# Performance work log

Measured on AMD Instinct MI355X. Metric: run time of the kernel, lower is better.

The kernel has to match this reference:

```python
import jax, jax.numpy as jnp
import numpy as np
import math

BS, SL, NE, NH = 4, 2048, 1024, 16
HD = NE // NH  # 64


def setup_inputs() -> dict:
    key = jax.random.key(0)
    ks = jax.random.split(key, 5)
    x = jax.random.normal(ks[0], (BS, SL, NE), dtype=jnp.float32)
    # causal mask: 1 where attending allowed (j <= i), 0 otherwise
    mask = jnp.tril(jnp.ones((SL, SL), dtype=jnp.int32))[None, None, :, :]
    s = 1.0 / math.sqrt(NE)
    Wqkv = jax.random.normal(ks[1], (NE, 3 * NE), dtype=jnp.float32) * s
    bqkv = jax.random.normal(ks[2], (3 * NE,), dtype=jnp.float32) * 0.02
    Wo = jax.random.normal(ks[3], (NE, NE), dtype=jnp.float32) * s
    bo = jax.random.normal(ks[4], (NE,), dtype=jnp.float32) * 0.02
    return {"x": x, "mask": mask, "Wqkv": Wqkv, "bqkv": bqkv, "Wo": Wo, "bo": bo}


def reference(x, mask, Wqkv, bqkv, Wo, bo):
    bs, sl, ne = x.shape
    qkv = x @ Wqkv + bqkv                       # [bs, sl, 3*ne]
    q, k, v = jnp.split(qkv, 3, axis=-1)
    # [bs, sl, ne] -> [bs, nh, sl, hd]
    q = q.reshape(bs, sl, NH, HD).transpose(0, 2, 1, 3)
    k = k.reshape(bs, sl, NH, HD).transpose(0, 2, 1, 3)
    v = v.reshape(bs, sl, NH, HD).transpose(0, 2, 1, 3)
    scale = 1.0 / math.sqrt(HD)
    att = jnp.einsum('bhqd,bhkd->bhqk', q, k) * scale  # [bs, nh, sl, sl]
    att = jnp.where(mask == 0, -jnp.inf, att)
    w = jax.nn.softmax(att, axis=-1)
    y = jnp.einsum('bhqk,bhkd->bhqd', w, v)            # [bs, nh, sl, hd]
    y = y.transpose(0, 2, 1, 3).reshape(bs, sl, ne)
    return y @ Wo + bo
```

## Files before the change

### kernel.cpp

```cpp
#include <hip/hip_runtime.h>

#define BS 4
#define SL 2048
#define NE 1024
#define NH 16
#define HD 64
#define N3 3072

typedef __attribute__((ext_vector_type(8))) __bf16 bf16x8;
typedef __attribute__((ext_vector_type(4))) float f32x4;
typedef __attribute__((ext_vector_type(4))) short s16x4;
typedef unsigned short u16;

#define CE 0.18033688011112042f

#if __has_builtin(__builtin_amdgcn_exp2f)
#define EXP2(x) __builtin_amdgcn_exp2f(x)
#else
#define EXP2(x) exp2f(x)
#endif

__device__ __forceinline__ u16 f2bf(float f) {
  union { float f; unsigned int u; } v; v.f = f;
  unsigned int r = v.u + 0x7FFFu + ((v.u >> 16) & 1u);
  return (u16)(r >> 16);
}

__device__ __forceinline__ int permpack(float a, float b) {
  return __builtin_amdgcn_perm(__float_as_uint(b), __float_as_uint(a),
                               0x07060302u);
}

__device__ __forceinline__ void gld16(const void* g, void* l) {
#if __has_builtin(__builtin_amdgcn_global_load_lds)
  __builtin_amdgcn_global_load_lds(
      (const __attribute__((address_space(1))) unsigned int*)g,
      (__attribute__((address_space(3))) unsigned int*)l, 16, 0, 0);
#else
  *(int4*)((char*)l + (size_t)(threadIdx.x & 63) * 16) = *(const int4*)g;
#endif
}

template <int N>
__device__ __forceinline__ void vmw() {
  if constexpr (N == 0)
    asm volatile("s_waitcnt vmcnt(0)" ::: "memory");
  else if constexpr (N == 4)
    asm volatile("s_waitcnt vmcnt(4)" ::: "memory");
}

__global__ void convert_x(const float* __restrict__ x, u16* __restrict__ xb) {
  int i = (blockIdx.x * 256 + threadIdx.x) * 8;
  float4 f0 = *(const float4*)(x + i);
  float4 f1 = *(const float4*)(x + i + 4);
  union { int4 v; u16 h[8]; } p;
  p.h[0] = f2bf(f0.x); p.h[1] = f2bf(f0.y);
  p.h[2] = f2bf(f0.z); p.h[3] = f2bf(f0.w);
  p.h[4] = f2bf(f1.x); p.h[5] = f2bf(f1.y);
  p.h[6] = f2bf(f1.z); p.h[7] = f2bf(f1.w);
  *(int4*)(xb + i) = p.v;
}

__global__ void transpose_w(const float* __restrict__ W, u16* __restrict__ Wt,
                            int K, int N) {
  __shared__ u16 tile[32][33];
  int bn = blockIdx.x * 32, bk = blockIdx.y * 32;
  int tx = threadIdx.x, ty = threadIdx.y;
  for (int r = 0; r < 32; r += 8)
    tile[ty + r][tx] = f2bf(W[(size_t)(bk + ty + r) * N + bn + tx]);
  __syncthreads();
  for (int r = 0; r < 32; r += 8)
    Wt[(size_t)(bn + ty + r) * K + bk + tx] = tile[tx][ty + r];
}

#define MFMA_G(a, b, c) \
  __builtin_amdgcn_mfma_f32_16x16x32_bf16(a, b, c, 0, 0, 0)
#define GBAR()                         \
  do {                                 \
    __builtin_amdgcn_s_barrier();      \
    __builtin_amdgcn_sched_barrier(0); \
  } while (0)

template <int C32, int SCALEQ>
__global__ __launch_bounds__(256, 3) void gemm3b(
    const u16* __restrict__ A, const u16* __restrict__ Bt,
    const float* __restrict__ bias, void* __restrict__ C, int M, int N, int K,
    int lda) {
  constexpr int BM = 128, BN = 128, BK = 32;
  constexpr int TSZ = BM * BK;
  __shared__ u16 As[3][TSZ];
  __shared__ u16 Bs[3][TSZ];

  const int tid = threadIdx.x;
  const int w = tid >> 6, lane = tid & 63;
  const int lq = lane >> 4, lr = lane & 15;
  const int nwx = gridDim.x;
  const int nwg = nwx * gridDim.y;
  const int lin = blockIdx.y * nwx + blockIdx.x;
  const int cpx = nwg >> 3;
  const int swb = (lin & 7) * cpx + (lin >> 3);
  const int m0 = (swb / nwx) * BM, n0 = (swb % nwx) * BN;
  const int wm = (w >> 1) * 64, wn = (w & 1) * 64;

  const int srow = lane >> 2;
  const int swcol = ((lane & 3) ^ ((lane >> 3) & 3)) * 8;
  const u16* gA = A + (size_t)(m0 + w * 32 + srow) * lda + swcol;
  const u16* gB = Bt + (size_t)(n0 + w * 32 + srow) * K + swcol;

#define STAGE3(abuf, bbuf, gpa, gpb)                          \
  do {                                                        \
    _Pragma("unroll") for (int c = 0; c < 2; c++) {           \
      gld16((gpa) + (size_t)(c * 16) * lda,                   \
            (abuf) + (w * 32 + c * 16) * 32);                 \
      gld16((gpb) + (size_t)(c * 16) * K,                     \
            (bbuf) + (w * 32 + c * 16) * 32);                 \
    }                                                         \
  } while (0)

  const f32x4 fzero = {0.f, 0.f, 0.f, 0.f};
  f32x4 acc[4][4];
#pragma unroll
  for (int i = 0; i < 4; i++)
#pragma unroll
    for (int j = 0; j < 4; j++) acc[i][j] = fzero;

  const int KT = K / BK;
  u16* asb = &As[0][0];
  u16* bsb = &Bs[0][0];
  STAGE3(asb, bsb, gA, gB);
  STAGE3(asb + TSZ, bsb + TSZ, gA + BK, gB + BK);
  vmw<4>();
  GBAR();
  const u16* gAn = gA + 2 * BK;
  const u16* gBn = gB + 2 * BK;

  int cur = 0, stg = 2;
  const int fswz = (lq ^ ((lr >> 1) & 3)) * 8;
  for (int T = 0; T < KT; T++) {
    if (T + 2 < KT) {
      STAGE3(asb + stg * TSZ, bsb + stg * TSZ, gAn, gBn);
      gAn += BK;
      gBn += BK;
    }
    __builtin_amdgcn_sched_barrier(0);

    const u16* Ac = asb + cur * TSZ;
    const u16* Bc = bsb + cur * TSZ;
    bf16x8 a[4], b[4];
#pragma unroll
    for (int i = 0; i < 4; i++)
      a[i] = *(const bf16x8*)&Ac[(wm + i * 16 + lr) * 32 + fswz];
#pragma unroll
    for (int j = 0; j < 4; j++)
      b[j] = *(const bf16x8*)&Bc[(wn + j * 16 + lr) * 32 + fswz];
    __builtin_amdgcn_s_setprio(1);
#pragma unroll
    for (int i = 0; i < 4; i++)
#pragma unroll
      for (int j = 0; j < 4; j++)
        acc[i][j] = MFMA_G(a[i], b[j], acc[i][j]);
    __builtin_amdgcn_s_setprio(0);

    if (T + 2 < KT) {
      vmw<4>();
      GBAR();
    } else if (T + 1 < KT) {
      vmw<0>();
      GBAR();
    }
    cur = (cur == 2) ? 0 : cur + 1;
    stg = (stg == 2) ? 0 : stg + 1;
  }
#undef STAGE3

#pragma unroll
  for (int j = 0; j < 4; j++) {
    int col = n0 + wn + j * 16 + lr;
    float bv = bias[col];
    float qs = (SCALEQ && col < NE) ? CE : 1.0f;
#pragma unroll
    for (int i = 0; i < 4; i++) {
#pragma unroll
      for (int r = 0; r < 4; r++) {
        int row = m0 + wm + i * 16 + lq * 4 + r;
        float val = acc[i][j][r] + bv;
        if (SCALEQ) val *= qs;
        if (C32) ((float*)C)[(size_t)row * N + col] = val;
        else     ((u16*)C)[(size_t)row * N + col]   = f2bf(val);
      }
    }
  }
}

#define KSTR 72
#define MFMA16(a, b, c) __builtin_amdgcn_mfma_f32_16x16x32_bf16(a, b, c, 0, 0, 0)
#define MFMA1616(a, b, c) \
  __builtin_amdgcn_mfma_f32_16x16x16bf16_1k(a, b, c, 0, 0, 0)

__device__ __forceinline__ void softmax_pack(f32x4 (&s)[4], s16x4 (&pa)[4],
                                             f32x4 (&o)[4], float& m_,
                                             float& l_) {
  float a0 = fmaxf(fmaxf(s[0][0], s[0][1]), s[0][2]);
  float a1 = fmaxf(fmaxf(s[0][3], s[1][0]), s[1][1]);
  float a2 = fmaxf(fmaxf(s[1][2], s[1][3]), s[2][0]);
  float a3 = fmaxf(fmaxf(s[2][1], s[2][2]), s[2][3]);
  float a4 = fmaxf(fmaxf(s[3][0], s[3][1]), s[3][2]);
  float mt = fmaxf(fmaxf(fmaxf(a0, a1), fmaxf(a2, a3)), fmaxf(a4, s[3][3]));
  mt = fmaxf(mt, __shfl_xor(mt, 16));
  mt = fmaxf(mt, __shfl_xor(mt, 32));
  bool need = !__all(mt <= m_ + 11.54f);
  float mn = need ? fmaxf(m_, mt) : m_;
  if (need) {
    float alpha = EXP2(m_ - mn);
    m_ = mn;
    l_ *= alpha;
#pragma unroll
    for (int jd = 0; jd < 4; jd++)
#pragma unroll
      for (int r = 0; r < 4; r++) o[jd][r] *= alpha;
  }
  float psum = 0.f;
#pragma unroll
  for (int j = 0; j < 4; j++) {
    float p0 = EXP2(s[j][0] - mn);
    float p1 = EXP2(s[j][1] - mn);
    float p2 = EXP2(s[j][2] - mn);
    float p3 = EXP2(s[j][3] - mn);
    psum += (p0 + p1) + (p2 + p3);
    union { int i[2]; s16x4 v; } pu;
    pu.i[0] = permpack(p0, p1);
    pu.i[1] = permpack(p2, p3);
    pa[j] = pu.v;
  }
  l_ += psum;
}

__device__ __forceinline__ void attn_step(const bf16x8& q0, const bf16x8& q1,
                                          const u16* __restrict__ Kb,
                                          const u16* __restrict__ Vb,
                                          bool diag, int qloc, int lq, int lr,
                                          f32x4 (&o)[4], float& m_, float& l_) {
  const f32x4 fzero = {0.f, 0.f, 0.f, 0.f};
  const int swz = (lq ^ ((lr >> 1) & 3)) * 8;
  f32x4 s[4];
  __builtin_amdgcn_s_setprio(1);
#pragma unroll
  for (int j = 0; j < 4; j++) {
    int kr = j * 16 + lr;
    bf16x8 kf0 = *(const bf16x8*)&Kb[kr * 32 + swz];
    bf16x8 kf1 = *(const bf16x8*)&Kb[2048 + kr * 32 + swz];
    f32x4 z = MFMA16(kf0, q0, fzero);
    s[j] = MFMA16(kf1, q1, z);
  }
  __builtin_amdgcn_s_setprio(0);
  if (diag) {
#pragma unroll
    for (int j = 0; j < 4; j++)
#pragma unroll
      for (int r = 0; r < 4; r++)
        if (16 * j + r > qloc) s[j][r] = -1e30f;
  }
  s16x4 pa[4];
  softmax_pack(s, pa, o, m_, l_);
  __builtin_amdgcn_s_setprio(1);
#pragma unroll
  for (int jd = 0; jd < 4; jd++) {
    const u16* vrow = &Vb[(jd * 16 + lr) * KSTR + lq * 16];
    union { int4 q; s16x4 h[2]; } va, vb;
    va.q = *(const int4*)vrow;
    vb.q = *(const int4*)(vrow + 8);
    o[jd] = MFMA1616(va.h[0], pa[0], o[jd]);
    o[jd] = MFMA1616(va.h[1], pa[1], o[jd]);
    o[jd] = MFMA1616(vb.h[0], pa[2], o[jd]);
    o[jd] = MFMA1616(vb.h[1], pa[3], o[jd]);
  }
  __builtin_amdgcn_s_setprio(0);
}

__global__ __launch_bounds__(256, 4) void attn_paired(u16* __restrict__ qkv) {
  __shared__ u16 Ks[2][4096];
  __shared__ u16 Vs[2][64 * KSTR];

  const int tid = threadIdx.x;
  const int w = tid >> 6, lane = tid & 63;
  const int lq = lane >> 4, lr = lane & 15;
  const int bh = blockIdx.x, p = blockIdx.y;
  const int h = bh & (NH - 1), b = bh >> 4;
  const int qt0 = p, qt1 = (SL / 64 - 1) - p;
  const int qloc = w * 16 + lr - 4 * lq;

  u16* base = qkv + (size_t)b * SL * N3;
  const u16* kbase = base + NE + h * HD;

  const int kg_key = lane >> 2;
  const int kg_blk = (lane & 3) ^ ((kg_key >> 1) & 3);
  const int sd0 = (tid >> 5) * 8;
  const int k0 = (tid & 31) * 2;
  const int k0p = ((k0 >> 2) & 3) * 16 + (k0 >> 4) * 4 + (k0 & 3);
  const u16* vrow0 = base + (size_t)k0 * N3 + 2 * NE + h * HD + sd0;

#define KPRE(buf, key0)                                                     \
  {                                                                         \
    _Pragma("unroll") for (int t = 0; t < 2; t++) {                         \
      int chunk = w * 2 + t, half = chunk >> 2, kgrp = chunk & 3;           \
      const u16* g = kbase + (size_t)((key0) + kgrp * 16 + kg_key) * N3 +   \
                     half * 32 + kg_blk * 8;                                \
      gld16(g, &Ks[buf][half * 2048 + kgrp * 512]);                         \
    }                                                                       \
  }
#define VWRITE(buf)                                                        \
  {                                                                        \
    union { int4 v; int d[4]; } t0, t1;                                    \
    t0.v = v0; t1.v = v1;                                                  \
    u16* Vn = &Vs[buf][0];                                                 \
    _Pragma("unroll") for (int dw = 0; dw < 4; dw++) {                     \
      int lo = __builtin_amdgcn_perm((unsigned)t1.d[dw],                   \
                                     (unsigned)t0.d[dw], 0x05040100u);     \
      int hi = __builtin_amdgcn_perm((unsigned)t1.d[dw],                   \
                                     (unsigned)t0.d[dw], 0x07060302u);     \
      *(int*)&Vn[(sd0 + 2 * dw) * KSTR + k0p] = lo;                        \
      *(int*)&Vn[(sd0 + 2 * dw + 1) * KSTR + k0p] = hi;                    \
    }                                                                      \
  }

  bf16x8 qf[2][2];
#pragma unroll
  for (int half = 0; half < 2; half++) {
    int qt = half ? qt1 : qt0;
    const u16* qrow = base + (size_t)(qt * 64 + w * 16 + lr) * N3 + h * HD;
    qf[half][0] = *(const bf16x8*)(qrow + lq * 8);
    qf[half][1] = *(const bf16x8*)(qrow + 32 + lq * 8);
  }

  const f32x4 fzero = {0.f, 0.f, 0.f, 0.f};
  f32x4 o[2][4];
  float m_[2], l_[2];
#pragma unroll
  for (int half = 0; half < 2; half++) {
    m_[half] = -1e30f;
    l_[half] = 0.f;
#pragma unroll
    for (int jd = 0; jd < 4; jd++) o[half][jd] = fzero;
  }

  KPRE(0, 0);
  int4 v0 = *(const int4*)vrow0;
  int4 v1 = *(const int4*)(vrow0 + N3);
  asm volatile("s_waitcnt vmcnt(0)" ::: "memory");
  VWRITE(0);
  {
    const u16* nv = vrow0 + (size_t)64 * N3;
    v0 = *(const int4*)nv;
    v1 = *(const int4*)(nv + N3);
  }

  const int ktend = qt1 + 1;
  for (int kt = 0; kt < ktend; kt++) {
    __syncthreads();
    const int nb = (kt + 1) & 1;
    if (kt + 1 < ktend) {
      KPRE(nb, (kt + 1) * 64);
      VWRITE(nb);
      if (kt + 2 < ktend) {
        const u16* nv = vrow0 + (size_t)(kt + 2) * 64 * N3;
        v0 = *(const int4*)nv;
        v1 = *(const int4*)(nv + N3);
      }
    }
    __builtin_amdgcn_sched_barrier(0);

    const u16* Kb = &Ks[kt & 1][0];
    const u16* Vb = &Vs[kt & 1][0];
    attn_step(qf[1][0], qf[1][1], Kb, Vb, kt == qt1, qloc, lq, lr, o[1], m_[1],
              l_[1]);
    if (kt <= qt0)
      attn_step(qf[0][0], qf[0][1], Kb, Vb, kt == qt0, qloc, lq, lr, o[0],
                m_[0], l_[0]);
  }

#pragma unroll
  for (int half = 0; half < 2; half++) {
    int qt = half ? qt1 : qt0;
    float lsum = l_[half];
    lsum += __shfl_xor(lsum, 16);
    lsum += __shfl_xor(lsum, 32);
    float inv = 1.0f / lsum;
    u16* yrow = base + (size_t)(qt * 64 + w * 16 + lr) * N3 + h * HD;
#pragma unroll
    for (int jd = 0; jd < 4; jd++) {
      int2 val;
      val.x = (int)(((unsigned)f2bf(o[half][jd][1] * inv) << 16) |
                    f2bf(o[half][jd][0] * inv));
      val.y = (int)(((unsigned)f2bf(o[half][jd][3] * inv) << 16) |
                    f2bf(o[half][jd][2] * inv));
      *(int2*)(yrow + 16 * jd + 4 * lq) = val;
    }
  }
}

extern "C" void kernel_launch(void* const* d_in, const int* in_sizes, int n_in,
                              void* d_out, int out_size, void* d_ws,
                              size_t ws_size, hipStream_t stream) {
  const float* x    = (const float*)d_in[0];
  const float* Wqkv = (const float*)d_in[2];
  const float* bqkv = (const float*)d_in[3];
  const float* Wo   = (const float*)d_in[4];
  const float* bo   = (const float*)d_in[5];

  u16* WqkvT  = (u16*)d_ws;
  u16* WoT    = WqkvT + (size_t)N3 * NE;
  u16* xb     = WoT + (size_t)NE * NE;
  u16* qkvbuf = xb + (size_t)BS * SL * NE;

  convert_x<<<(BS * SL * NE) / (256 * 8), 256, 0, stream>>>(x, xb);
  transpose_w<<<dim3(N3 / 32, NE / 32), dim3(32, 8), 0, stream>>>(Wqkv, WqkvT,
                                                                  NE, N3);
  transpose_w<<<dim3(NE / 32, NE / 32), dim3(32, 8), 0, stream>>>(Wo, WoT, NE,
                                                                  NE);
  gemm3b<0, 1><<<dim3(N3 / 128, (BS * SL) / 128), 256, 0, stream>>>(
      xb, WqkvT, bqkv, qkvbuf, BS * SL, N3, NE, NE);
  attn_paired<<<dim3(BS * NH, SL / 128), 256, 0, stream>>>(qkvbuf);
  gemm3b<1, 0><<<dim3(NE / 128, (BS * SL) / 128), 256, 0, stream>>>(
      qkvbuf, WoT, bo, d_out, BS * SL, NE, NE, N3);
}
```

Baseline: 259.8 us.

## Fuse prep kernels into one launch and deepen GEMM pipeline to four stages

The three preprocessing kernels (x conversion and two weight transposes) are merged into a single launch that dispatches on block index, removing two kernel launches. The GEMM moves from a 3-stage to a 4-stage LDS ring buffer with three tiles prefetched ahead. Launch bounds drop from 3 to 2 workgroups per SM to fit the larger LDS footprint. This trades occupancy for deeper latency hiding of global loads.

```diff
diff --git a/kernel.cpp b/kernel.cpp
--- a/kernel.cpp
+++ b/kernel.cpp
@@ -47,25 +47,40 @@
     asm volatile("s_waitcnt vmcnt(0)" ::: "memory");
   else if constexpr (N == 4)
     asm volatile("s_waitcnt vmcnt(4)" ::: "memory");
-}
-
-__global__ void convert_x(const float* __restrict__ x, u16* __restrict__ xb) {
-  int i = (blockIdx.x * 256 + threadIdx.x) * 8;
-  float4 f0 = *(const float4*)(x + i);
-  float4 f1 = *(const float4*)(x + i + 4);
-  union { int4 v; u16 h[8]; } p;
-  p.h[0] = f2bf(f0.x); p.h[1] = f2bf(f0.y);
-  p.h[2] = f2bf(f0.z); p.h[3] = f2bf(f0.w);
-  p.h[4] = f2bf(f1.x); p.h[5] = f2bf(f1.y);
-  p.h[6] = f2bf(f1.z); p.h[7] = f2bf(f1.w);
-  *(int4*)(xb + i) = p.v;
-}
-
-__global__ void transpose_w(const float* __restrict__ W, u16* __restrict__ Wt,
-                            int K, int N) {
+  else if constexpr (N == 8)
+    asm volatile("s_waitcnt vmcnt(8)" ::: "memory");
+}
+
+__global__ void prep(const float* __restrict__ x, u16* __restrict__ xb,
+                     const float* __restrict__ Wqkv, u16* __restrict__ WqkvT,
+                     const float* __restrict__ Wo, u16* __restrict__ WoT) {
   __shared__ u16 tile[32][33];
-  int bn = blockIdx.x * 32, bk = blockIdx.y * 32;
-  int tx = threadIdx.x, ty = threadIdx.y;
+  const int bid = blockIdx.x, tid = threadIdx.x;
+  if (bid < 4096) {
+    int i = (bid * 256 + tid) * 8;
+    float4 f0 = *(const float4*)(x + i);
+    float4 f1 = *(const float4*)(x + i + 4);
+    union { int4 v; u16 h[8]; } p;
+    p.h[0] = f2bf(f0.x); p.h[1] = f2bf(f0.y);
+    p.h[2] = f2bf(f0.z); p.h[3] = f2bf(f0.w);
+    p.h[4] = f2bf(f1.x); p.h[5] = f2bf(f1.y);
+    p.h[6] = f2bf(f1.z); p.h[7] = f2bf(f1.w);
+    *(int4*)(xb + i) = p.v;
+    return;
+  }
+  const float* W;
+  u16* Wt;
+  int K, N, tb;
+  if (bid < 7168) {
+    tb = bid - 4096;
+    W = Wqkv; Wt = WqkvT; K = NE; N = N3;
+  } else {
+    tb = bid - 7168;
+    W = Wo; Wt = WoT; K = NE; N = NE;
+  }
+  const int ntx = N / 32;
+  const int bn = (tb % ntx) * 32, bk = (tb / ntx) * 32;
+  const int tx = tid & 31, ty = tid >> 5;
   for (int r = 0; r < 32; r += 8)
     tile[ty + r][tx] = f2bf(W[(size_t)(bk + ty + r) * N + bn + tx]);
   __syncthreads();
@@ -82,14 +97,14 @@
   } while (0)
 
 template <int C32, int SCALEQ>
-__global__ __launch_bounds__(256, 3) void gemm3b(
+__global__ __launch_bounds__(256, 2) void gemm4b(
     const u16* __restrict__ A, const u16* __restrict__ Bt,
     const float* __restrict__ bias, void* __restrict__ C, int M, int N, int K,
     int lda) {
   constexpr int BM = 128, BN = 128, BK = 32;
   constexpr int TSZ = BM * BK;
-  __shared__ u16 As[3][TSZ];
-  __shared__ u16 Bs[3][TSZ];
+  __shared__ u16 As[4][TSZ];
+  __shared__ u16 Bs[4][TSZ];
 
   const int tid = threadIdx.x;
   const int w = tid >> 6, lane = tid & 63;
@@ -107,13 +122,13 @@
   const u16* gA = A + (size_t)(m0 + w * 32 + srow) * lda + swcol;
   const u16* gB = Bt + (size_t)(n0 + w * 32 + srow) * K + swcol;
 
-#define STAGE3(abuf, bbuf, gpa, gpb)                          \
+#define STAGE4(buf, gpa, gpb)                                 \
   do {                                                        \
     _Pragma("unroll") for (int c = 0; c < 2; c++) {           \
       gld16((gpa) + (size_t)(c * 16) * lda,                   \
-            (abuf) + (w * 32 + c * 16) * 32);                 \
+            &As[buf][(w * 32 + c * 16) * 32]);                \
       gld16((gpb) + (size_t)(c * 16) * K,                     \
-            (bbuf) + (w * 32 + c * 16) * 32);                 \
+            &Bs[buf][(w * 32 + c * 16) * 32]);                \
     }                                                         \
   } while (0)
 
@@ -125,27 +140,27 @@
     for (int j = 0; j < 4; j++) acc[i][j] = fzero;
 
   const int KT = K / BK;
-  u16* asb = &As[0][0];
-  u16* bsb = &Bs[0][0];
-  STAGE3(asb, bsb, gA, gB);
-  STAGE3(asb + TSZ, bsb + TSZ, gA + BK, gB + BK);
-  vmw<4>();
+  STAGE4(0, gA, gB);
+  STAGE4(1, gA + BK, gB + BK);
+  STAGE4(2, gA + 2 * BK, gB + 2 * BK);
+  vmw<8>();
   GBAR();
-  const u16* gAn = gA + 2 * BK;
-  const u16* gBn = gB + 2 * BK;
-
-  int cur = 0, stg = 2;
+  const u16* gAn = gA + 3 * BK;
+  const u16* gBn = gB + 3 * BK;
+
   const int fswz = (lq ^ ((lr >> 1) & 3)) * 8;
   for (int T = 0; T < KT; T++) {
-    if (T + 2 < KT) {
-      STAGE3(asb + stg * TSZ, bsb + stg * TSZ, gAn, gBn);
+    const int cur = T & 3;
+    const bool pf = (T + 3 < KT);
+    if (pf) {
+      STAGE4((T + 3) & 3, gAn, gBn);
       gAn += BK;
       gBn += BK;
     }
     __builtin_amdgcn_sched_barrier(0);
 
-    const u16* Ac = asb + cur * TSZ;
-    const u16* Bc = bsb + cur * TSZ;
+    const u16* Ac = &As[cur][0];
+    const u16* Bc = &Bs[cur][0];
     bf16x8 a[4], b[4];
 #pragma unroll
     for (int i = 0; i < 4; i++)
@@ -161,17 +176,18 @@
         acc[i][j] = MFMA_G(a[i], b[j], acc[i][j]);
     __builtin_amdgcn_s_setprio(0);
 
-    if (T + 2 < KT) {
+    if (pf) {
+      vmw<8>();
+      GBAR();
+    } else if (T + 2 < KT) {
       vmw<4>();
       GBAR();
     } else if (T + 1 < KT) {
       vmw<0>();
       GBAR();
     }
-    cur = (cur == 2) ? 0 : cur + 1;
-    stg = (stg == 2) ? 0 : stg + 1;
-  }
-#undef STAGE3
+  }
+#undef STAGE4
 
 #pragma unroll
   for (int j = 0; j < 4; j++) {
@@ -412,14 +428,10 @@
   u16* xb     = WoT + (size_t)NE * NE;
   u16* qkvbuf = xb + (size_t)BS * SL * NE;
 
-  convert_x<<<(BS * SL * NE) / (256 * 8), 256, 0, stream>>>(x, xb);
-  transpose_w<<<dim3(N3 / 32, NE / 32), dim3(32, 8), 0, stream>>>(Wqkv, WqkvT,
-                                                                  NE, N3);
-  transpose_w<<<dim3(NE / 32, NE / 32), dim3(32, 8), 0, stream>>>(Wo, WoT, NE,
-                                                                  NE);
-  gemm3b<0, 1><<<dim3(N3 / 128, (BS * SL) / 128), 256, 0, stream>>>(
+  prep<<<8192, 256, 0, stream>>>(x, xb, Wqkv, WqkvT, Wo, WoT);
+  gemm4b<0, 1><<<dim3(N3 / 128, (BS * SL) / 128), 256, 0, stream>>>(
       xb, WqkvT, bqkv, qkvbuf, BS * SL, N3, NE, NE);
   attn_paired<<<dim3(BS * NH, SL / 128), 256, 0, stream>>>(qkvbuf);
-  gemm3b<1, 0><<<dim3(NE / 128, (BS * SL) / 128), 256, 0, stream>>>(
+  gemm4b<1, 0><<<dim3(NE / 128, (BS * SL) / 128), 256, 0, stream>>>(
       qkvbuf, WoT, bo, d_out, BS * SL, NE, NE, N3);
 }
```

Measured after the change: 269.3 us. 3.7% more time.
